# Optimization experiments

Hardware: AMD Instinct MI355X
Metric: run time of the kernel (lower is better)

## Reference

```python
import jax, jax.numpy as jnp
import numpy as np

EPS = 1e-8

def render_point_cloud(xyz, data, h, w):
    """Soft z-buffer splatting: nearest-pixel scatter with inverse-depth weights.
    xyz: (bs, p, 3) NDC coords; data: (bs, c, p). Returns (bs,c,h,w), (bs,1,h,w), (bs,p) bool."""
    bs, c, p = data.shape
    x = (xyz[..., 0] + 1.0) * 0.5 * (w - 1)   # NDC -> pixel coords
    y = (xyz[..., 1] + 1.0) * 0.5 * (h - 1)
    z = xyz[..., 2]
    viz = (x > -0.5) & (x < w - 0.5) & (y > -0.5) & (y < h - 0.5) & (z > 0)  # (bs,p)
    xi = jnp.clip(jnp.round(x), 0, w - 1).astype(jnp.int32)
    yi = jnp.clip(jnp.round(y), 0, h - 1).astype(jnp.int32)
    # inverse-depth confidence weight; invisible points contribute nothing
    wgt = jnp.where(viz, 1.0 / jnp.maximum(z, EPS), 0.0)  # (bs,p)
    pix = yi * w + xi                                      # (bs,p)
    seg = (jnp.arange(bs, dtype=jnp.int32)[:, None] * (h * w) + pix).reshape(-1)  # (bs*p,)
    feat = (data * wgt[:, None, :]).transpose(0, 2, 1).reshape(bs * p, c)
    acc = jax.ops.segment_sum(feat, seg, num_segments=bs * h * w)          # (bs*h*w, c)
    conf = jax.ops.segment_sum(wgt.reshape(-1), seg, num_segments=bs * h * w)
    acc = acc.reshape(bs, h, w, c).transpose(0, 3, 1, 2)   # (bs,c,h,w)
    conf = conf.reshape(bs, 1, h, w)
    out = acc / jnp.maximum(conf, EPS)                     # weight-normalized splat
    return out, conf, viz


def setup_inputs() -> dict:
    key = jax.random.key(0)
    k1, k2, k3 = jax.random.split(key, 3)
    bs, p, c, h, w = 4, 262144, 32, 512, 512
    xy = jax.random.uniform(k1, (bs, p, 2), dtype=jnp.float32, minval=-1.05, maxval=1.05)
    z = jax.random.uniform(k2, (bs, p, 1), dtype=jnp.float32, minval=0.5, maxval=5.0)
    xyz = jnp.concatenate([xy, z], axis=-1)               # (bs,p,3)
    data = jax.random.normal(k3, (bs, c, p), dtype=jnp.float32)
    return {"xyz": xyz, "data": data, "h": h, "w": w}


def reference(xyz, data, h, w):
    assert xyz.shape[1] == data.shape[2]
    out, conf, viz = render_point_cloud(xyz, data, h, w)
    return out, conf, viz
```

## Files before the change

### kernel.cpp

```cpp
#include <hip/hip_runtime.h>

#define BS 4
#define P  262144
#define C  32
#define H  512
#define W  512
#define HW (H * W)
#define NEPS 1e-8f


#define TP 64

__device__ inline void pk_add_bf16(unsigned short* p, unsigned int v)
{
    asm volatile("global_atomic_pk_add_bf16 %0, %1, off"
                 :: "v"(p), "v"(v) : "memory");
}

__device__ inline unsigned int pack_bf16_rne(float a, float b)
{
    unsigned int ua = __builtin_bit_cast(unsigned int, a);
    unsigned int ub = __builtin_bit_cast(unsigned int, b);
    ua += 0x7FFFu + ((ua >> 16) & 1u);
    ub += 0x7FFFu + ((ub >> 16) & 1u);
    return (ua >> 16) | (ub & 0xFFFF0000u);
}

__global__ __launch_bounds__(256) void splat_scatter_t(
    const float* __restrict__ xyz, const float* __restrict__ data,
    unsigned short* __restrict__ acc, float* __restrict__ conf,
    float* __restrict__ viz)
{
    __shared__ float s_feat[C][TP + 1];
    __shared__ float s_xyz[TP * 3];
    __shared__ float s_wgt[TP];
    __shared__ int   s_pix[TP];

    const int t     = threadIdx.x;
    const int chunk = blockIdx.x;
    const int base  = chunk * TP;
    const int b     = base >> 18;
    const int j0    = base & (P - 1);

    const float4* dsrc = (const float4*)(data + (size_t)b * C * P + j0);
    #pragma unroll
    for (int i = 0; i < 2; ++i) {
        int f4 = i * 256 + t;
        int ch = f4 >> 4;
        int q  = f4 & 15;
        float4 v = dsrc[(size_t)ch * (P / 4) + q];
        s_feat[ch][q * 4 + 0] = v.x;
        s_feat[ch][q * 4 + 1] = v.y;
        s_feat[ch][q * 4 + 2] = v.z;
        s_feat[ch][q * 4 + 3] = v.w;
    }
    if (t < 48) {
        float4 v = ((const float4*)(xyz + (size_t)base * 3))[t];
        s_xyz[t * 4 + 0] = v.x;
        s_xyz[t * 4 + 1] = v.y;
        s_xyz[t * 4 + 2] = v.z;
        s_xyz[t * 4 + 3] = v.w;
    }
    __syncthreads();

    if (t < TP) {
        float x = s_xyz[3 * t + 0];
        float y = s_xyz[3 * t + 1];
        float z = s_xyz[3 * t + 2];
        float px = (x + 1.0f) * 0.5f * (float)(W - 1);
        float py = (y + 1.0f) * 0.5f * (float)(H - 1);
        bool v = (px > -0.5f) && (px < (float)W - 0.5f) &&
                 (py > -0.5f) && (py < (float)H - 0.5f) && (z > 0.0f);
        viz[base + t] = v ? 1.0f : 0.0f;
        int pix = -1;
        float wg = 0.0f;
        if (v) {
            int xi = (int)fminf(fmaxf(rintf(px), 0.0f), (float)(W - 1));
            int yi = (int)fminf(fmaxf(rintf(py), 0.0f), (float)(H - 1));
            pix = yi * W + xi;
            wg  = 1.0f / fmaxf(z, NEPS);
            unsafeAtomicAdd(&conf[b * HW + pix], wg);
        }
        s_pix[t] = pix;
        s_wgt[t] = wg;
    }
    __syncthreads();

    const int g  = t >> 4;
    const int c2 = t & 15;
    #pragma unroll
    for (int k = 0; k < TP / 16; ++k) {
        int jj  = k * 16 + g;
        int pix = s_pix[jj];
        if (pix >= 0) {
            float wg = s_wgt[jj];
            float a0 = s_feat[2 * c2 + 0][jj] * wg;
            float a1 = s_feat[2 * c2 + 1][jj] * wg;
            pk_add_bf16(acc + (((size_t)b << 18) + pix) * C + 2 * c2,
                        pack_bf16_rne(a0, a1));
        }
    }
}

__global__ __launch_bounds__(256) void splat_transpose_norm(
    const unsigned short* __restrict__ acc, const float* __restrict__ conf,
    float* __restrict__ out)
{
    __shared__ float s_t[TP][C + 1];
    __shared__ float s_inv[TP];

    const int t    = threadIdx.x;
    const int blk  = blockIdx.x;
    const int b    = blk >> (18 - 6);
    const int pix0 = (blk & ((HW / TP) - 1)) * TP;

    if (t < TP)
        s_inv[t] = 1.0f / fmaxf(conf[(size_t)b * HW + pix0 + t], NEPS);

    const uint4* src = (const uint4*)(acc + ((size_t)b * HW + pix0) * C);
    {
        uint4 v = src[t];
        int po  = t >> 2;
        int ch0 = (t & 3) * 8;
        unsigned int ws[4] = {v.x, v.y, v.z, v.w};
        #pragma unroll
        for (int w = 0; w < 4; ++w) {
            unsigned int lo = (ws[w] & 0xFFFFu) << 16;
            unsigned int hi = ws[w] & 0xFFFF0000u;
            s_t[po][ch0 + 2 * w + 0] = __builtin_bit_cast(float, lo);
            s_t[po][ch0 + 2 * w + 1] = __builtin_bit_cast(float, hi);
        }
    }
    __syncthreads();

    #pragma unroll
    for (int i = 0; i < 8; ++i) {
        int e  = i * 256 + t;
        int ch = e >> 6;
        int po = e & 63;
        out[((size_t)b * C + ch) * HW + pix0 + po] = s_t[po][ch] * s_inv[po];
    }
}


__global__ __launch_bounds__(256) void splat_scatter_fb(
    const float* __restrict__ xyz, const float* __restrict__ data,
    float* __restrict__ acc, float* __restrict__ conf, float* __restrict__ viz)
{
    int idx = blockIdx.x * 256 + threadIdx.x;
    if (idx >= BS * P) return;
    int b = idx >> 18;
    int j = idx & (P - 1);
    float x = xyz[3 * idx + 0], y = xyz[3 * idx + 1], z = xyz[3 * idx + 2];
    float px = (x + 1.0f) * 0.5f * (float)(W - 1);
    float py = (y + 1.0f) * 0.5f * (float)(H - 1);
    bool v = (px > -0.5f) && (px < (float)W - 0.5f) &&
             (py > -0.5f) && (py < (float)H - 0.5f) && (z > 0.0f);
    viz[idx] = v ? 1.0f : 0.0f;
    if (!v) return;
    int xi = (int)fminf(fmaxf(rintf(px), 0.0f), (float)(W - 1));
    int yi = (int)fminf(fmaxf(rintf(py), 0.0f), (float)(H - 1));
    float wg = 1.0f / fmaxf(z, NEPS);
    int pix = yi * W + xi;
    unsafeAtomicAdd(&conf[b * HW + pix], wg);
    const float* db = data + (size_t)b * C * P + j;
    float*       ab = acc  + (size_t)b * C * HW + pix;
    #pragma unroll
    for (int ch = 0; ch < C; ++ch)
        unsafeAtomicAdd(ab + (size_t)ch * HW, db[(size_t)ch * P] * wg);
}

__global__ __launch_bounds__(256) void splat_norm_fb(
    float* __restrict__ out, const float* __restrict__ conf)
{
    int idx = blockIdx.x * 256 + threadIdx.x;
    if (idx >= BS * HW) return;
    int b   = idx >> 18;
    int pix = idx & (HW - 1);
    float inv = 1.0f / fmaxf(conf[idx], NEPS);
    float* ob = out + (size_t)b * C * HW + pix;
    #pragma unroll
    for (int ch = 0; ch < C; ++ch)
        ob[(size_t)ch * HW] *= inv;
}

extern "C" void kernel_launch(void* const* d_in, const int* in_sizes, int n_in,
                              void* d_out, int out_size, void* d_ws, size_t ws_size,
                              hipStream_t stream)
{
    const float* xyz  = (const float*)d_in[0];
    const float* data = (const float*)d_in[1];

    float* out  = (float*)d_out;
    float* conf = out  + (size_t)BS * C * HW;
    float* viz  = conf + (size_t)BS * HW;

    const size_t acc_bytes = (size_t)BS * HW * C * sizeof(unsigned short);

    if (ws_size >= acc_bytes) {
        unsigned short* acc = (unsigned short*)d_ws;
        (void)hipMemsetAsync(acc, 0, acc_bytes, stream);
        (void)hipMemsetAsync(conf, 0, (size_t)BS * HW * sizeof(float), stream);
        splat_scatter_t<<<BS * P / TP, 256, 0, stream>>>(xyz, data, acc, conf, viz);
        splat_transpose_norm<<<BS * HW / TP, 256, 0, stream>>>(acc, conf, out);
    } else {
        (void)hipMemsetAsync(d_out, 0, (size_t)(BS * C * HW + BS * HW) * sizeof(float), stream);
        splat_scatter_fb<<<(BS * P + 255) / 256, 256, 0, stream>>>(xyz, data, out, conf, viz);
        splat_norm_fb<<<(BS * HW + 255) / 256, 256, 0, stream>>>(out, conf);
    }
}
```

Before: 150.9 us.

## Enlarge scatter tile to 256 points and stage features as packed bf16

The scatter kernel now processes 256 points per block instead of 64, so all threads compute visibility and weights and the block count drops fourfold. Feature data is converted to packed bf16 pairs when staged into shared memory, which halves LDS footprint and read traffic, and the weight multiply runs on the unpacked values. The extra early rounding to bf16 before weighting adds a second rounding step and may shift accuracy slightly. The transpose kernel is decoupled from TP and keeps its 64-pixel tiles.

Result: no change. 151.3 us (+0.3%).

```diff
diff --git a/kernel.cpp b/kernel.cpp
--- a/kernel.cpp
+++ b/kernel.cpp
@@ -9,7 +9,8 @@
 #define NEPS 1e-8f
 
 
-#define TP 64
+#define TP 256
+#define SPAD (TP + 4)
 
 __device__ inline void pk_add_bf16(unsigned short* p, unsigned int v)
 {
@@ -25,45 +26,50 @@
     ub += 0x7FFFu + ((ub >> 16) & 1u);
     return (ua >> 16) | (ub & 0xFFFF0000u);
 }
+__device__ inline float bf16_lo(unsigned int w) { return __builtin_bit_cast(float, w << 16); }
+__device__ inline float bf16_hi(unsigned int w) { return __builtin_bit_cast(float, w & 0xFFFF0000u); }
 
 __global__ __launch_bounds__(256) void splat_scatter_t(
     const float* __restrict__ xyz, const float* __restrict__ data,
     unsigned short* __restrict__ acc, float* __restrict__ conf,
     float* __restrict__ viz)
 {
-    __shared__ float s_feat[C][TP + 1];
+    __shared__ __align__(16) unsigned int s_pk[C / 2][SPAD];
     __shared__ float s_xyz[TP * 3];
     __shared__ float s_wgt[TP];
     __shared__ int   s_pix[TP];
 
-    const int t     = threadIdx.x;
-    const int chunk = blockIdx.x;
-    const int base  = chunk * TP;
-    const int b     = base >> 18;
-    const int j0    = base & (P - 1);
-
-    const float4* dsrc = (const float4*)(data + (size_t)b * C * P + j0);
-    #pragma unroll
-    for (int i = 0; i < 2; ++i) {
-        int f4 = i * 256 + t;
-        int ch = f4 >> 4;
-        int q  = f4 & 15;
-        float4 v = dsrc[(size_t)ch * (P / 4) + q];
-        s_feat[ch][q * 4 + 0] = v.x;
-        s_feat[ch][q * 4 + 1] = v.y;
-        s_feat[ch][q * 4 + 2] = v.z;
-        s_feat[ch][q * 4 + 3] = v.w;
-    }
-    if (t < 48) {
+    const int t    = threadIdx.x;
+    const int base = blockIdx.x * TP;
+    const int b    = base >> 18;
+    const int j0   = base & (P - 1);
+
+    if (t < 192) {
         float4 v = ((const float4*)(xyz + (size_t)base * 3))[t];
         s_xyz[t * 4 + 0] = v.x;
         s_xyz[t * 4 + 1] = v.y;
         s_xyz[t * 4 + 2] = v.z;
         s_xyz[t * 4 + 3] = v.w;
     }
+
+    const float4* dsrc = (const float4*)(data + (size_t)b * C * P + j0);
+    #pragma unroll
+    for (int i = 0; i < 4; ++i) {
+        int e = i * 256 + t;
+        int c = e >> 6;
+        int q = e & 63;
+        float4 va = dsrc[(size_t)(2 * c + 0) * (P / 4) + q];
+        float4 vb = dsrc[(size_t)(2 * c + 1) * (P / 4) + q];
+        uint4 r;
+        r.x = pack_bf16_rne(va.x, vb.x);
+        r.y = pack_bf16_rne(va.y, vb.y);
+        r.z = pack_bf16_rne(va.z, vb.z);
+        r.w = pack_bf16_rne(va.w, vb.w);
+        *(uint4*)&s_pk[c][4 * q] = r;
+    }
     __syncthreads();
 
-    if (t < TP) {
+    {
         float x = s_xyz[3 * t + 0];
         float y = s_xyz[3 * t + 1];
         float z = s_xyz[3 * t + 2];
@@ -86,18 +92,17 @@
     }
     __syncthreads();
 
-    const int g  = t >> 4;
-    const int c2 = t & 15;
+    const int g = t >> 4;
+    const int d = t & 15;
     #pragma unroll
     for (int k = 0; k < TP / 16; ++k) {
         int jj  = k * 16 + g;
         int pix = s_pix[jj];
         if (pix >= 0) {
             float wg = s_wgt[jj];
-            float a0 = s_feat[2 * c2 + 0][jj] * wg;
-            float a1 = s_feat[2 * c2 + 1][jj] * wg;
-            pk_add_bf16(acc + (((size_t)b << 18) + pix) * C + 2 * c2,
-                        pack_bf16_rne(a0, a1));
+            unsigned int pk = s_pk[d][jj];
+            pk_add_bf16(acc + (((size_t)b << 18) + pix) * C + 2 * d,
+                        pack_bf16_rne(bf16_lo(pk) * wg, bf16_hi(pk) * wg));
         }
     }
 }
@@ -106,15 +111,15 @@
     const unsigned short* __restrict__ acc, const float* __restrict__ conf,
     float* __restrict__ out)
 {
-    __shared__ float s_t[TP][C + 1];
-    __shared__ float s_inv[TP];
+    __shared__ float s_t[64][C + 1];
+    __shared__ float s_inv[64];
 
     const int t    = threadIdx.x;
     const int blk  = blockIdx.x;
-    const int b    = blk >> (18 - 6);
-    const int pix0 = (blk & ((HW / TP) - 1)) * TP;
-
-    if (t < TP)
+    const int b    = blk >> 12;
+    const int pix0 = (blk & ((HW / 64) - 1)) * 64;
+
+    if (t < 64)
         s_inv[t] = 1.0f / fmaxf(conf[(size_t)b * HW + pix0 + t], NEPS);
 
     const uint4* src = (const uint4*)(acc + ((size_t)b * HW + pix0) * C);
@@ -125,10 +130,8 @@
         unsigned int ws[4] = {v.x, v.y, v.z, v.w};
         #pragma unroll
         for (int w = 0; w < 4; ++w) {
-            unsigned int lo = (ws[w] & 0xFFFFu) << 16;
-            unsigned int hi = ws[w] & 0xFFFF0000u;
-            s_t[po][ch0 + 2 * w + 0] = __builtin_bit_cast(float, lo);
-            s_t[po][ch0 + 2 * w + 1] = __builtin_bit_cast(float, hi);
+            s_t[po][ch0 + 2 * w + 0] = bf16_lo(ws[w]);
+            s_t[po][ch0 + 2 * w + 1] = bf16_hi(ws[w]);
         }
     }
     __syncthreads();
@@ -202,7 +205,7 @@
         (void)hipMemsetAsync(acc, 0, acc_bytes, stream);
         (void)hipMemsetAsync(conf, 0, (size_t)BS * HW * sizeof(float), stream);
         splat_scatter_t<<<BS * P / TP, 256, 0, stream>>>(xyz, data, acc, conf, viz);
-        splat_transpose_norm<<<BS * HW / TP, 256, 0, stream>>>(acc, conf, out);
+        splat_transpose_norm<<<BS * HW / 64, 256, 0, stream>>>(acc, conf, out);
     } else {
         (void)hipMemsetAsync(d_out, 0, (size_t)(BS * C * HW + BS * HW) * sizeof(float), stream);
         splat_scatter_fb<<<(BS * P + 255) / 256, 256, 0, stream>>>(xyz, data, out, conf, viz);
```
